# Kernel optimization log

Hardware: AMD Instinct MI355X
Metric: run time of the kernel (lower is better)

The kernel has to match this reference:

```python
import jax, jax.numpy as jnp
import numpy as np

H = 20   # num heads
D = 64   # head dim (hidden_size=1280)
N_IMG = 4
N_LBL = 4
SCALE_IMG = 1.0
SCALE_LBL = 1.0


def setup_inputs() -> dict:
    key = jax.random.key(0)
    ks = jax.random.split(key, 12)
    B, S, C, Dc = 4, 4096, 1280, 2048
    L = 77 + N_IMG + N_LBL  # 85 encoder tokens
    w = lambda k, shp: jax.random.normal(k, shp, dtype=jnp.float32) * 0.02
    return {
        "hidden_states": jax.random.normal(ks[0], (B, S, C), dtype=jnp.float32),
        "encoder_hidden_states": jax.random.normal(ks[1], (B, L, Dc), dtype=jnp.float32),
        "Wq": w(ks[2], (C, C)),
        "Wk": w(ks[3], (Dc, C)),
        "Wv": w(ks[4], (Dc, C)),
        "Wk_ip": w(ks[5], (Dc, C)),
        "Wv_ip": w(ks[6], (Dc, C)),
        "Wk_lbl": w(ks[7], (Dc, C)),
        "Wv_lbl": w(ks[8], (Dc, C)),
        "Wo": w(ks[9], (C, C)),
        "bo": jnp.zeros((C,), dtype=jnp.float32),
    }


def _attend(q, enc, Wk_, Wv_):
    # q: [B, S, H, D]; enc: [B, L, Dc]
    B, L = enc.shape[0], enc.shape[1]
    k = (enc @ Wk_).reshape(B, L, H, D)
    v = (enc @ Wv_).reshape(B, L, H, D)
    scores = jnp.einsum("bqhd,bkhd->bhqk", q, k) * (D ** -0.5)
    p = jax.nn.softmax(scores, axis=-1)
    return jnp.einsum("bhqk,bkhd->bqhd", p, v)


def reference(hidden_states, encoder_hidden_states, Wq, Wk, Wv,
              Wk_ip, Wv_ip, Wk_lbl, Wv_lbl, Wo, bo):
    B, S, C = hidden_states.shape
    end = encoder_hidden_states.shape[1] - N_IMG - N_LBL
    enc_text = encoder_hidden_states[:, :end]
    enc_img = encoder_hidden_states[:, end:end + N_IMG]
    enc_lbl = encoder_hidden_states[:, end + N_IMG:]

    q = (hidden_states @ Wq).reshape(B, S, H, D)

    out = _attend(q, enc_text, Wk, Wv)
    out = out + SCALE_IMG * _attend(q, enc_img, Wk_ip, Wv_ip)
    out = out + SCALE_LBL * _attend(q, enc_lbl, Wk_lbl, Wv_lbl)

    out = out.reshape(B, S, C) @ Wo + bo
    return out + hidden_states  # residual_connection=True, rescale=1.0
```

## Files before the change

### kernel.cpp

```cpp
#include <hip/hip_runtime.h>
#include <hip/hip_bf16.h>

typedef unsigned short u16;
using f32x4  = __attribute__((ext_vector_type(4))) float;
using bf16x8 = __attribute__((ext_vector_type(8))) short;

#define N_B 4
#define N_S 4096
#define N_C 1280
#define N_DC 2048
#define N_H 20
#define N_D 64

__device__ __forceinline__ u16 f2b(float f) {
  union { float f; unsigned u; } x; x.f = f;
  return (u16)((x.u + 0x7fffu + ((x.u >> 16) & 1u)) >> 16);
}

__device__ __forceinline__ void gld16(const u16* g, u16* l) {
  __builtin_amdgcn_global_load_lds(
      (const __attribute__((address_space(1))) unsigned int*)(g),
      (__attribute__((address_space(3))) unsigned int*)(l), 16, 0, 0);
}

__global__ void k_cvt(const float* __restrict__ src, u16* __restrict__ dst, int n8) {
  for (int i = blockIdx.x * 256 + threadIdx.x; i < n8; i += gridDim.x * 256) {
    const float4 v0 = *(const float4*)(src + (size_t)i * 8);
    const float4 v1 = *(const float4*)(src + (size_t)i * 8 + 4);
    alignas(16) u16 t[8];
    t[0] = f2b(v0.x); t[1] = f2b(v0.y); t[2] = f2b(v0.z); t[3] = f2b(v0.w);
    t[4] = f2b(v1.x); t[5] = f2b(v1.y); t[6] = f2b(v1.z); t[7] = f2b(v1.w);
    *(uint4*)(dst + (size_t)i * 8) = *(uint4*)t;
  }
}

struct TPargs { const float* s[8]; u16* d[8]; int K[8]; };

__global__ void k_transpose8(TPargs a) {
  int z = blockIdx.z;
  const float* __restrict__ src = a.s[z];
  u16* __restrict__ dst = a.d[z];
  int K = a.K[z];
  int k0 = blockIdx.y * 32;
  if (k0 >= K) return;
  __shared__ float tl[32][33];
  int n0 = blockIdx.x * 32;
  int tx = threadIdx.x, ty = threadIdx.y;
#pragma unroll
  for (int j = 0; j < 32; j += 8)
    tl[ty + j][tx] = src[(size_t)(k0 + ty + j) * N_C + (n0 + tx)];
  __syncthreads();
#pragma unroll
  for (int j = 0; j < 32; j += 8)
    dst[(size_t)(n0 + ty + j) * K + (k0 + tx)] = f2b(tl[tx][ty + j]);
}

__global__ void k_encpack(const float* __restrict__ enc, u16* __restrict__ txt,
                          u16* __restrict__ img, u16* __restrict__ lbl) {
  int row = blockIdx.x;
  int b = row / 85, l = row % 85;
  const float* s = enc + (size_t)row * N_DC;
  u16* d;
  if (l < 77)      d = txt + (size_t)(b * 77 + l) * N_DC;
  else if (l < 81) d = img + (size_t)(b * 4 + (l - 77)) * N_DC;
  else             d = lbl + (size_t)(b * 4 + (l - 81)) * N_DC;
  for (int i = threadIdx.x; i < N_DC; i += 256) d[i] = f2b(s[i]);
}


__device__ __forceinline__ void stage64(const u16* __restrict__ g, int ldK,
                                        int row0, int kk, u16* ldsb,
                                        int w, int lane) {
  int r = w * 8 + (lane >> 3);
  int gslot = ((lane & 7) ^ (lane >> 3)) << 3;
  gld16(g + (size_t)(row0 + r) * ldK + kk + gslot, ldsb + w * 512);
}
__device__ __forceinline__ void stageA4(const u16* Ag, int K, int kk, u16* ldsb,
                                        int w, int lane) {
#pragma unroll
  for (int j = 0; j < 4; j++)
    stage64(Ag, K, j * 64, kk, ldsb + j * 4096, w, lane);
}
__device__ __forceinline__ void stageB5(const u16* Bg, int K, int kk, u16* ldsb,
                                        int w, int lane) {
#pragma unroll
  for (int j = 0; j < 5; j++)
    stage64(Bg, K, j * 64, kk, ldsb + j * 4096, w, lane);
}

#define RD_A2(aoff, mh)                                                      \
  _Pragma("unroll") for (int mi = 0; mi < 2; mi++) {                         \
    _Pragma("unroll") for (int ks = 0; ks < 2; ks++) {                       \
      int row = wr * 128 + ((mh) * 2 + mi) * 16 + lrow;                      \
      int slot = (ks * 4 + g) ^ (lane & 7);                                  \
      af[mi][ks] = *(const bf16x8*)&lds[(aoff) + row * 64 + slot * 8];       \
    }                                                                        \
  }

#define RD_B5(boff)                                                          \
  _Pragma("unroll") for (int n = 0; n < 5; n++) {                            \
    _Pragma("unroll") for (int ks = 0; ks < 2; ks++) {                       \
      int row = wc * 80 + n * 16 + lrow;                                     \
      int slot = (ks * 4 + g) ^ (lane & 7);                                  \
      bf[n][ks] = *(const bf16x8*)&lds[(boff) + row * 64 + slot * 8];        \
    }                                                                        \
  }

#define MFMA20(mh)                                                           \
  _Pragma("unroll") for (int mi = 0; mi < 2; mi++) {                         \
    _Pragma("unroll") for (int n = 0; n < 5; n++) {                          \
      _Pragma("unroll") for (int ks = 0; ks < 2; ks++)                       \
        acc[(mh) * 2 + mi][n] = __builtin_amdgcn_mfma_f32_16x16x32_bf16(     \
            af[mi][ks], bf[n][ks], acc[(mh) * 2 + mi][n], 0, 0, 0);          \
    }                                                                        \
  }

#define BARR()  __builtin_amdgcn_s_barrier()
#define VM0()   asm volatile("s_waitcnt vmcnt(0)" ::: "memory")
#define PRIO(x) __builtin_amdgcn_s_setprio(x)

template<int EPI>
__global__ __launch_bounds__(512, 1)
void gemm8p(const u16* __restrict__ A, const u16* __restrict__ Bt,
            void* __restrict__ Cv, int M, int N, int K, float scale,
            const float* __restrict__ bias, const float* __restrict__ resid) {
  __shared__ __align__(16) u16 lds[73728];
  const int t = threadIdx.x, lane = t & 63, w = t >> 6;
  const int wr = w >> 2, wc = w & 3;
  const int lrow = lane & 15, g = lane >> 4;

  int nt = N / 320;
  int nwg = gridDim.x, bid = blockIdx.x;
  int swz = ((nwg & 7) == 0) ? ((bid & 7) * (nwg >> 3) + (bid >> 3)) : bid;
  int bm = swz / nt, bn = swz % nt;

  const u16* Ag = A  + (size_t)bm * 256 * K;
  const u16* Bg = Bt + (size_t)bn * 320 * K;
  const int NT = K >> 6;

  f32x4 acc[8][5] = {};
  bf16x8 af[2][2], bf[5][2];

  stageA4(Ag, K, 0, lds + 0,     w, lane);
  stageB5(Bg, K, 0, lds + 32768, w, lane);
  VM0();
  BARR();

  for (int tt = 0; tt < NT; ++tt) {
    int c = tt & 1;
    int aof  = c * 16384,        bof  = 32768 + c * 20480;
    int aof1 = (c ^ 1) * 16384,  bof1 = 32768 + (c ^ 1) * 20480;
    if (tt + 1 < NT) {
      stageA4(Ag, K, (tt + 1) * 64, lds + aof1, w, lane);
      stageB5(Bg, K, (tt + 1) * 64, lds + bof1, w, lane);
    }
    RD_A2(aof, 0); RD_B5(bof);
    PRIO(1); MFMA20(0); PRIO(0);
    RD_A2(aof, 1);
    PRIO(1); MFMA20(1); PRIO(0);
    RD_A2(aof, 2);
    PRIO(1); MFMA20(2); PRIO(0);
    RD_A2(aof, 3);
    PRIO(1); MFMA20(3); PRIO(0);
    VM0();
    BARR();
  }

#pragma unroll
  for (int m = 0; m < 8; m++) {
    int row = bm * 256 + wr * 128 + m * 16 + g * 4;
#pragma unroll
    for (int n = 0; n < 5; n++) {
      int col = bn * 320 + wc * 80 + n * 16 + lrow;
#pragma unroll
      for (int j = 0; j < 4; j++) {
        float v = acc[m][n][j];
        if constexpr (EPI == 1)
          ((u16*)Cv)[(size_t)(row + j) * N + col] = f2b(v * scale);
        else
          ((float*)Cv)[(size_t)(row + j) * N + col] =
              v + bias[col] + resid[(size_t)(row + j) * N + col];
      }
    }
  }
}

__global__ __launch_bounds__(256, 2)
void kv_gemm(const u16* __restrict__ etxt, const u16* __restrict__ eimg, const u16* __restrict__ elbl,
             const u16* __restrict__ wk,   const u16* __restrict__ wv,
             const u16* __restrict__ wkip, const u16* __restrict__ wvip,
             const u16* __restrict__ wklb, const u16* __restrict__ wvlb,
             u16* ktxt, u16* vtxt, u16* kimg, u16* vimg, u16* klbl, u16* vlbl) {
  __shared__ __align__(16) u16 lds[2][2][8192];
  int bn = blockIdx.x, my = blockIdx.y, kv = blockIdx.z;
  const u16 *A, *Bt; u16* C; int M, bm;
  if (my < 3)       { A = etxt; M = 308; bm = my; Bt = kv ? wv   : wk;   C = kv ? vtxt : ktxt; }
  else if (my == 3) { A = eimg; M = 16;  bm = 0;  Bt = kv ? wvip : wkip; C = kv ? vimg : kimg; }
  else              { A = elbl; M = 16;  bm = 0;  Bt = kv ? wvlb : wklb; C = kv ? vlbl : klbl; }
  const int K = 2048;
  int t = threadIdx.x, lane = t & 63, w = t >> 6;
  int wm = w >> 1, wn = w & 1;
  int c8 = lane & 7, rsub = lane >> 3;

  f32x4 acc[4][4] = {};

#define KVSTAGE(kt, buf)                                                      \
  {                                                                           \
    int k0 = (kt) * 64;                                                       \
    _Pragma("unroll") for (int i2 = 0; i2 < 4; i2++) {                        \
      int rloc = w * 32 + i2 * 8;                                             \
      int ra = bm * 128 + rloc + rsub; if (ra >= M) ra = M - 1;               \
      int rb = bn * 128 + rloc + rsub;                                        \
      gld16(A  + (size_t)ra * K + k0 + c8 * 8, &lds[buf][0][rloc * 64]);      \
      gld16(Bt + (size_t)rb * K + k0 + c8 * 8, &lds[buf][1][rloc * 64]);      \
    }                                                                         \
  }

  KVSTAGE(0, 0);
  asm volatile("s_waitcnt vmcnt(0)" ::: "memory");
  __syncthreads();
  int cur = 0;
  for (int kt = 0; kt < 32; kt++) {
    if (kt < 31) KVSTAGE(kt + 1, cur ^ 1);
#pragma unroll
    for (int ks = 0; ks < 2; ks++) {
      bf16x8 afr[4], bfr[4];
#pragma unroll
      for (int m = 0; m < 4; m++)
        afr[m] = *(bf16x8*)&lds[cur][0][(wm * 64 + m * 16 + (lane & 15)) * 64 + ks * 32 + (lane >> 4) * 8];
#pragma unroll
      for (int n = 0; n < 4; n++)
        bfr[n] = *(bf16x8*)&lds[cur][1][(wn * 64 + n * 16 + (lane & 15)) * 64 + ks * 32 + (lane >> 4) * 8];
#pragma unroll
      for (int m = 0; m < 4; m++)
#pragma unroll
        for (int n = 0; n < 4; n++)
          acc[m][n] = __builtin_amdgcn_mfma_f32_16x16x32_bf16(afr[m], bfr[n], acc[m][n], 0, 0, 0);
    }
    asm volatile("s_waitcnt vmcnt(0)" ::: "memory");
    __syncthreads();
    cur ^= 1;
  }
#undef KVSTAGE

#pragma unroll
  for (int m = 0; m < 4; m++) {
    int row = bm * 128 + wm * 64 + m * 16 + ((lane >> 4) << 2);
#pragma unroll
    for (int n = 0; n < 4; n++) {
      int col = bn * 128 + wn * 64 + n * 16 + (lane & 15);
#pragma unroll
      for (int j = 0; j < 4; j++) {
        int r = row + j;
        if (r >= M) continue;
        ((u16*)C)[(size_t)r * 1280 + col] = f2b(acc[m][n][j]);
      }
    }
  }
}

#define QSTR 72
#define PSTR 104

__global__ __launch_bounds__(256, 2)
void attn_kern(const u16* __restrict__ q,
               const u16* __restrict__ ktxt, const u16* __restrict__ vtxt,
               const u16* __restrict__ kimg, const u16* __restrict__ vimg,
               const u16* __restrict__ klbl, const u16* __restrict__ vlbl,
               u16* __restrict__ outa) {
  __shared__ __align__(16) char smem[45568];
  u16* Qs = (u16*)smem;
  u16* Ks = (u16*)(smem + 18432);
  u16* Ps = (u16*)smem;
  u16* Vt = (u16*)(smem + 32256);

  int st = blockIdx.x, h = blockIdx.y, b = blockIdx.z;
  int t = threadIdx.x, lane = t & 63, w = t >> 6;
  int s0 = st * 128;
  int c = lane & 15, g = lane >> 4;

  for (int i = t; i < 27136 / 16; i += 256)
    ((uint4*)(smem + 18432))[i] = make_uint4(0, 0, 0, 0);
#pragma unroll
  for (int i = 0; i < 4; i++) {
    int cid = t + i * 256; int r = cid >> 3, c8 = cid & 7;
    *(uint4*)&Qs[r * QSTR + c8 * 8] =
        *(const uint4*)(q + (size_t)(b * N_S + s0 + r) * N_C + h * N_D + c8 * 8);
  }
  __syncthreads();
  for (int cid = t; cid < 680; cid += 256) {
    int l = cid >> 3, c8 = cid & 7;
    const u16* p;
    if (l < 77)      p = ktxt + (size_t)(b * 77 + l) * N_C + h * N_D + c8 * 8;
    else if (l < 81) p = kimg + (size_t)(b * 4 + l - 77) * N_C + h * N_D + c8 * 8;
    else             p = klbl + (size_t)(b * 4 + l - 81) * N_C + h * N_D + c8 * 8;
    int row = (l < 77) ? l : l + 3;
    *(uint4*)&Ks[row * QSTR + c8 * 8] = *(const uint4*)p;
  }
  for (int e = t; e < 85 * 64; e += 256) {
    int l = e >> 6, d = e & 63;
    const u16* p;
    if (l < 77)      p = vtxt + (size_t)(b * 77 + l) * N_C + h * N_D + d;
    else if (l < 81) p = vimg + (size_t)(b * 4 + l - 77) * N_C + h * N_D + d;
    else             p = vlbl + (size_t)(b * 4 + l - 81) * N_C + h * N_D + d;
    int slot = (l < 77) ? l : l + 3;
    Vt[d * PSTR + slot] = *p;
  }
  __syncthreads();

  f32x4 sacc[2][6] = {};
#pragma unroll
  for (int ks = 0; ks < 2; ks++) {
    bf16x8 aq[2], bk[6];
#pragma unroll
    for (int m = 0; m < 2; m++)
      aq[m] = *(bf16x8*)&Qs[(w * 32 + m * 16 + c) * QSTR + ks * 32 + g * 8];
#pragma unroll
    for (int n = 0; n < 6; n++)
      bk[n] = *(bf16x8*)&Ks[(n * 16 + c) * QSTR + ks * 32 + g * 8];
#pragma unroll
    for (int m = 0; m < 2; m++)
#pragma unroll
      for (int n = 0; n < 6; n++)
        sacc[m][n] = __builtin_amdgcn_mfma_f32_16x16x32_bf16(aq[m], bk[n], sacc[m][n], 0, 0, 0);
  }
  __syncthreads();

  const float NEG = -1e30f;
#pragma unroll
  for (int m = 0; m < 2; m++) {
#pragma unroll
    for (int j = 0; j < 4; j++) {
      float tmax = NEG;
#pragma unroll
      for (int n = 0; n < 5; n++)
        if (n * 16 + c < 77) tmax = fmaxf(tmax, sacc[m][n][j]);
#pragma unroll
      for (int off = 1; off < 16; off <<= 1) tmax = fmaxf(tmax, __shfl_xor(tmax, off));
      float pv[5], tsum = 0.f;
#pragma unroll
      for (int n = 0; n < 5; n++) {
        float v = (n * 16 + c < 77) ? __expf(sacc[m][n][j] - tmax) : 0.f;
        pv[n] = v; tsum += v;
      }
#pragma unroll
      for (int off = 1; off < 16; off <<= 1) tsum += __shfl_xor(tsum, off);
      float v5 = sacc[m][5][j];
      float imax = (c < 4) ? v5 : NEG;
#pragma unroll
      for (int off = 1; off < 16; off <<= 1) imax = fmaxf(imax, __shfl_xor(imax, off));
      float ie = (c < 4) ? __expf(v5 - imax) : 0.f, isum = ie;
#pragma unroll
      for (int off = 1; off < 16; off <<= 1) isum += __shfl_xor(isum, off);
      float lmax = (c >= 4 && c < 8) ? v5 : NEG;
#pragma unroll
      for (int off = 1; off < 16; off <<= 1) lmax = fmaxf(lmax, __shfl_xor(lmax, off));
      float le = (c >= 4 && c < 8) ? __expf(v5 - lmax) : 0.f, lsum = le;
#pragma unroll
      for (int off = 1; off < 16; off <<= 1) lsum += __shfl_xor(lsum, off);

      float rt = 1.f / tsum;
      float p5 = (c < 4) ? ie / isum : ((c < 8) ? le / lsum : 0.f);
      int rowl = w * 32 + m * 16 + g * 4 + j;
#pragma unroll
      for (int n = 0; n < 5; n++)
        Ps[rowl * PSTR + n * 16 + c] = f2b(pv[n] * rt);
      Ps[rowl * PSTR + 80 + c] = f2b(p5);
    }
  }
  __syncthreads();

  f32x4 oacc[2][4] = {};
#pragma unroll
  for (int ks = 0; ks < 3; ks++) {
    bf16x8 ap[2], bv[4];
#pragma unroll
    for (int m = 0; m < 2; m++)
      ap[m] = *(bf16x8*)&Ps[(w * 32 + m * 16 + c) * PSTR + ks * 32 + g * 8];
#pragma unroll
    for (int n = 0; n < 4; n++)
      bv[n] = *(bf16x8*)&Vt[(n * 16 + c) * PSTR + ks * 32 + g * 8];
#pragma unroll
    for (int m = 0; m < 2; m++)
#pragma unroll
      for (int n = 0; n < 4; n++)
        oacc[m][n] = __builtin_amdgcn_mfma_f32_16x16x32_bf16(ap[m], bv[n], oacc[m][n], 0, 0, 0);
  }

#pragma unroll
  for (int m = 0; m < 2; m++) {
    int rbase = w * 32 + m * 16 + g * 4;
#pragma unroll
    for (int n = 0; n < 4; n++) {
      int d = n * 16 + c;
#pragma unroll
      for (int j = 0; j < 4; j++) {
        int s = s0 + rbase + j;
        outa[(size_t)(b * N_S + s) * N_C + h * N_D + d] = f2b(oacc[m][n][j]);
      }
    }
  }
}

extern "C" void kernel_launch(void* const* d_in, const int* in_sizes, int n_in,
                              void* d_out, int out_size, void* d_ws, size_t ws_size,
                              hipStream_t stream) {
  const float* hs   = (const float*)d_in[0];
  const float* enc  = (const float*)d_in[1];
  const float* Wq   = (const float*)d_in[2];
  const float* Wk   = (const float*)d_in[3];
  const float* Wv   = (const float*)d_in[4];
  const float* Wkip = (const float*)d_in[5];
  const float* Wvip = (const float*)d_in[6];
  const float* Wklb = (const float*)d_in[7];
  const float* Wvlb = (const float*)d_in[8];
  const float* Wo   = (const float*)d_in[9];
  const float* bo   = (const float*)d_in[10];

  if (ws_size < 83087360u) return;
  char* ws = (char*)d_ws;
  u16* wq_t   = (u16*)(ws + 0);
  u16* wo_t   = (u16*)(ws + 3276800);
  u16* wk_t   = (u16*)(ws + 6553600);
  u16* wv_t   = (u16*)(ws + 11796480);
  u16* wkip_t = (u16*)(ws + 17039360);
  u16* wvip_t = (u16*)(ws + 22282240);
  u16* wklb_t = (u16*)(ws + 27525120);
  u16* wvlb_t = (u16*)(ws + 32768000);
  u16* etxt   = (u16*)(ws + 38010880);
  u16* eimg   = (u16*)(ws + 39272448);
  u16* elbl   = (u16*)(ws + 39337984);
  u16* ktxt   = (u16*)(ws + 39403520);
  u16* vtxt   = (u16*)(ws + 40192000);
  u16* kimg   = (u16*)(ws + 40980480);
  u16* vimg   = (u16*)(ws + 41021440);
  u16* klbl   = (u16*)(ws + 41062400);
  u16* vlbl   = (u16*)(ws + 41103360);
  u16* attn   = (u16*)(ws + 41144320);
  u16* qbuf   = (u16*)d_out;
  u16* hsb    = (u16*)d_out + (size_t)N_S * N_B * N_C;

  k_cvt<<<2048, 256, 0, stream>>>(hs, hsb, (N_B * N_S * N_C) / 8);

  TPargs tp;
  tp.s[0] = Wq;   tp.d[0] = wq_t;   tp.K[0] = 1280;
  tp.s[1] = Wo;   tp.d[1] = wo_t;   tp.K[1] = 1280;
  tp.s[2] = Wk;   tp.d[2] = wk_t;   tp.K[2] = 2048;
  tp.s[3] = Wv;   tp.d[3] = wv_t;   tp.K[3] = 2048;
  tp.s[4] = Wkip; tp.d[4] = wkip_t; tp.K[4] = 2048;
  tp.s[5] = Wvip; tp.d[5] = wvip_t; tp.K[5] = 2048;
  tp.s[6] = Wklb; tp.d[6] = wklb_t; tp.K[6] = 2048;
  tp.s[7] = Wvlb; tp.d[7] = wvlb_t; tp.K[7] = 2048;
  k_transpose8<<<dim3(40, 64, 8), dim3(32, 8), 0, stream>>>(tp);

  k_encpack<<<340, 256, 0, stream>>>(enc, etxt, eimg, elbl);

  gemm8p<1><<<256, 512, 0, stream>>>(hsb, wq_t, qbuf, 16384, 1280, 1280,
                                     0.125f, nullptr, nullptr);
  kv_gemm<<<dim3(10, 5, 2), 256, 0, stream>>>(etxt, eimg, elbl,
                                              wk_t, wv_t, wkip_t, wvip_t, wklb_t, wvlb_t,
                                              ktxt, vtxt, kimg, vimg, klbl, vlbl);

  attn_kern<<<dim3(32, N_H, N_B), 256, 0, stream>>>(qbuf, ktxt, vtxt, kimg, vimg,
                                                    klbl, vlbl, attn);
  gemm8p<2><<<256, 512, 0, stream>>>(attn, wo_t, d_out, 16384, 1280, 1280,
                                     1.f, bo, hs);
}
```

Measured before the change: 257.7 us.

## Load GEMM B operand directly from global into registers, dropping its LDS staging

The B tile is no longer staged through shared memory. Each wave now loads its own B fragments straight from global memory into registers at the start of every k-step, and LDS shrinks to just the double-buffered A tile. The aim is to cut LDS traffic and footprint for B. In exchange, the B loads are unpipelined global reads issued immediately before the MFMAs, and waves sharing a column block read the same B data redundantly, so latency may be exposed.

```diff
diff --git a/kernel.cpp b/kernel.cpp
--- a/kernel.cpp
+++ b/kernel.cpp
@@ -81,12 +81,6 @@
   for (int j = 0; j < 4; j++)
     stage64(Ag, K, j * 64, kk, ldsb + j * 4096, w, lane);
 }
-__device__ __forceinline__ void stageB5(const u16* Bg, int K, int kk, u16* ldsb,
-                                        int w, int lane) {
-#pragma unroll
-  for (int j = 0; j < 5; j++)
-    stage64(Bg, K, j * 64, kk, ldsb + j * 4096, w, lane);
-}
 
 #define RD_A2(aoff, mh)                                                      \
   _Pragma("unroll") for (int mi = 0; mi < 2; mi++) {                         \
@@ -97,15 +91,6 @@
     }                                                                        \
   }
 
-#define RD_B5(boff)                                                          \
-  _Pragma("unroll") for (int n = 0; n < 5; n++) {                            \
-    _Pragma("unroll") for (int ks = 0; ks < 2; ks++) {                       \
-      int row = wc * 80 + n * 16 + lrow;                                     \
-      int slot = (ks * 4 + g) ^ (lane & 7);                                  \
-      bf[n][ks] = *(const bf16x8*)&lds[(boff) + row * 64 + slot * 8];        \
-    }                                                                        \
-  }
-
 #define MFMA20(mh)                                                           \
   _Pragma("unroll") for (int mi = 0; mi < 2; mi++) {                         \
     _Pragma("unroll") for (int n = 0; n < 5; n++) {                          \
@@ -124,7 +109,7 @@
 void gemm8p(const u16* __restrict__ A, const u16* __restrict__ Bt,
             void* __restrict__ Cv, int M, int N, int K, float scale,
             const float* __restrict__ bias, const float* __restrict__ resid) {
-  __shared__ __align__(16) u16 lds[73728];
+  __shared__ __align__(16) u16 lds[32768];
   const int t = threadIdx.x, lane = t & 63, w = t >> 6;
   const int wr = w >> 2, wc = w & 3;
   const int lrow = lane & 15, g = lane >> 4;
@@ -135,26 +120,27 @@
   int bm = swz / nt, bn = swz % nt;
 
   const u16* Ag = A  + (size_t)bm * 256 * K;
-  const u16* Bg = Bt + (size_t)bn * 320 * K;
+  const u16* Bl = Bt + (size_t)(bn * 320 + wc * 80 + lrow) * K + g * 8;
   const int NT = K >> 6;
 
   f32x4 acc[8][5] = {};
   bf16x8 af[2][2], bf[5][2];
 
-  stageA4(Ag, K, 0, lds + 0,     w, lane);
-  stageB5(Bg, K, 0, lds + 32768, w, lane);
+  stageA4(Ag, K, 0, lds + 0, w, lane);
   VM0();
   BARR();
 
   for (int tt = 0; tt < NT; ++tt) {
     int c = tt & 1;
-    int aof  = c * 16384,        bof  = 32768 + c * 20480;
-    int aof1 = (c ^ 1) * 16384,  bof1 = 32768 + (c ^ 1) * 20480;
-    if (tt + 1 < NT) {
-      stageA4(Ag, K, (tt + 1) * 64, lds + aof1, w, lane);
-      stageB5(Bg, K, (tt + 1) * 64, lds + bof1, w, lane);
-    }
-    RD_A2(aof, 0); RD_B5(bof);
+    int aof  = c * 16384;
+    int aof1 = (c ^ 1) * 16384;
+#pragma unroll
+    for (int n = 0; n < 5; n++)
+#pragma unroll
+      for (int ks = 0; ks < 2; ks++)
+        bf[n][ks] = *(const bf16x8*)(Bl + (size_t)n * 16 * K + tt * 64 + ks * 32);
+    if (tt + 1 < NT) stageA4(Ag, K, (tt + 1) * 64, lds + aof1, w, lane);
+    RD_A2(aof, 0);
     PRIO(1); MFMA20(0); PRIO(0);
     RD_A2(aof, 1);
     PRIO(1); MFMA20(1); PRIO(0);
```

Result: slower. 321.3 us (+24.7%).
